# Performance work log

Hardware: AMD Instinct MI355X
Metric: run time of the kernel (lower is better)

## Reference

```python
import jax, jax.numpy as jnp
import numpy as np

N_USER, N_ITEM, N_REL = 200000, 100000, 64
DIM = 64
S_UU = S_UI = S_IU = S_II = 8
BATCH = 65536
MAX_RATING = 5.0


def setup_inputs() -> dict:
    key = jax.random.key(0)
    ks = jax.random.split(key, 24)
    inp = {}
    # query batch
    inp['u'] = jax.random.randint(ks[0], (BATCH,), 0, N_USER)
    inp['v'] = jax.random.randint(ks[1], (BATCH,), 0, N_ITEM)
    # embedding tables (init std=0.8 as in the torch code)
    inp['usr_feat'] = 0.8 * jax.random.normal(ks[2], (N_USER, DIM), jnp.float32)
    inp['item_feat'] = 0.8 * jax.random.normal(ks[3], (N_ITEM, DIM), jnp.float32)
    inp['rel_feat'] = 0.8 * jax.random.normal(ks[4], (N_REL, DIM), jnp.float32)
    # precomputed sampled neighbor tables (built once in __init__ in the original)
    inp['neigh_uu'] = jax.random.randint(ks[5], (N_USER, S_UU), 0, N_USER)
    inp['neigh_uu_st'] = jax.random.uniform(ks[6], (N_USER, S_UU), jnp.float32)
    inp['neigh_ui'] = jax.random.randint(ks[7], (N_USER, S_UI), 0, N_ITEM)
    inp['neigh_ui_rat'] = MAX_RATING * jax.random.uniform(ks[8], (N_USER, S_UI), jnp.float32)
    inp['neigh_ui_vot'] = jax.random.uniform(ks[9], (N_USER, S_UI), jnp.float32)
    inp['neigh_ui_tim'] = jax.random.uniform(ks[10], (N_USER, S_UI), jnp.float32)
    inp['neigh_iu'] = jax.random.randint(ks[11], (N_ITEM, S_IU), 0, N_USER)
    inp['neigh_iu_rat'] = MAX_RATING * jax.random.uniform(ks[12], (N_ITEM, S_IU), jnp.float32)
    inp['neigh_iu_vot'] = jax.random.uniform(ks[13], (N_ITEM, S_IU), jnp.float32)
    inp['neigh_iu_tim'] = jax.random.uniform(ks[14], (N_ITEM, S_IU), jnp.float32)
    inp['neigh_ii'] = jax.random.randint(ks[15], (N_ITEM, S_II), 0, N_ITEM)
    inp['neigh_ir'] = jax.random.randint(ks[16], (N_ITEM, S_II), 0, N_REL)
    # aggregator transforms (one per side)
    sc = 1.0 / np.sqrt(DIM)
    inp['Wu'] = sc * jax.random.normal(ks[17], (DIM, DIM), jnp.float32)
    inp['bu'] = jnp.zeros((DIM,), jnp.float32)
    inp['Wv'] = sc * jax.random.normal(ks[18], (DIM, DIM), jnp.float32)
    inp['bv'] = jnp.zeros((DIM,), jnp.float32)
    return inp


def reference(u, v, usr_feat, item_feat, rel_feat,
              neigh_uu, neigh_uu_st, neigh_ui, neigh_ui_rat, neigh_ui_vot, neigh_ui_tim,
              neigh_iu, neigh_iu_rat, neigh_iu_vot, neigh_iu_tim, neigh_ii, neigh_ir,
              Wu, bu, Wv, bv):
    u_emb = usr_feat[u]                                   # [B, D]
    v_emb = item_feat[v]                                  # [B, D]

    # ---- user-side aggregation ----
    # social neighbors, weighted by softmax over social tie strength
    uu_nei = usr_feat[neigh_uu[u]]                        # [B, S, D]
    w_uu = jax.nn.softmax(neigh_uu_st[u], axis=-1)        # [B, S]
    agg_uu = jnp.einsum('bs,bsd->bd', w_uu, uu_nei)
    # interacted items, weighted by rating * vote * time recency
    ui_nei = item_feat[neigh_ui[u]]                       # [B, S, D]
    s_ui = neigh_ui_rat[u] * neigh_ui_vot[u] * neigh_ui_tim[u]
    w_ui = jax.nn.softmax(s_ui, axis=-1)
    agg_ui = jnp.einsum('bs,bsd->bd', w_ui, ui_nei)
    user_h = jax.nn.relu((u_emb + agg_uu + agg_ui) @ Wu + bu)

    # ---- item-side aggregation ----
    # users who interacted with the item, weighted like above
    iu_nei = usr_feat[neigh_iu[v]]                        # [B, S, D]
    s_iu = neigh_iu_rat[v] * neigh_iu_vot[v] * neigh_iu_tim[v]
    w_iu = jax.nn.softmax(s_iu, axis=-1)
    agg_iu = jnp.einsum('bs,bsd->bd', w_iu, iu_nei)
    # KG neighbors with user-relation attention (KGCN-style)
    ii_nei = item_feat[neigh_ii[v]]                       # [B, S, D]
    rel = rel_feat[neigh_ir[v]]                           # [B, S, D]
    att = jnp.einsum('bd,bsd->bs', u_emb, rel)            # user-relation score
    w_ii = jax.nn.softmax(att, axis=-1)
    agg_ii = jnp.einsum('bs,bsd->bd', w_ii, ii_nei)
    item_h = jax.nn.relu((v_emb + agg_iu + agg_ii) @ Wv + bv)

    # rating prediction
    score = jax.nn.sigmoid(jnp.sum(user_h * item_h, axis=-1)) * MAX_RATING
    return score
```

## Files before the change

### kernel.cpp

```cpp
#include <hip/hip_runtime.h>
#include <math.h>

constexpr int DIM = 64;
constexpr int S = 8;
constexpr int WPB = 8;
constexpr int BLOCK = WPB * 64;
constexpr int GRID = 1024;
constexpr int WSTR = 68;

__device__ __forceinline__ void octet_softmax(float sc, float* wout) {
    float m = sc;
    m = fmaxf(m, __shfl_xor(m, 1));
    m = fmaxf(m, __shfl_xor(m, 2));
    m = fmaxf(m, __shfl_xor(m, 4));
    float e = __expf(sc - m);
    float s = e;
    s += __shfl_xor(s, 1);
    s += __shfl_xor(s, 2);
    s += __shfl_xor(s, 4);
    float w = e / s;
    #pragma unroll
    for (int k = 0; k < 8; k++) wout[k] = __shfl(w, k);
}

__global__ __launch_bounds__(BLOCK)
void sestkgcn_kernel(
    const int*   __restrict__ u_idx,
    const int*   __restrict__ v_idx,
    const float* __restrict__ usr_feat,
    const float* __restrict__ item_feat,
    const float* __restrict__ rel_feat,
    const int*   __restrict__ neigh_uu,
    const float* __restrict__ neigh_uu_st,
    const int*   __restrict__ neigh_ui,
    const float* __restrict__ neigh_ui_rat,
    const float* __restrict__ neigh_ui_vot,
    const float* __restrict__ neigh_ui_tim,
    const int*   __restrict__ neigh_iu,
    const float* __restrict__ neigh_iu_rat,
    const float* __restrict__ neigh_iu_vot,
    const float* __restrict__ neigh_iu_tim,
    const int*   __restrict__ neigh_ii,
    const int*   __restrict__ neigh_ir,
    const float* __restrict__ Wu,
    const float* __restrict__ bu,
    const float* __restrict__ Wv,
    const float* __restrict__ bv,
    float*       __restrict__ out,
    int n)
{
    __shared__ float sWuT[DIM * WSTR];
    __shared__ float sWvT[DIM * WSTR];
    __shared__ float sbu[DIM];
    __shared__ float sbv[DIM];
    __shared__ float xs[WPB * DIM];

    const int tid = threadIdx.x;
    for (int i = tid; i < DIM * DIM; i += BLOCK) {
        const int d_ = i >> 6, j_ = i & 63;
        sWuT[j_ * WSTR + d_] = Wu[i];
        sWvT[j_ * WSTR + d_] = Wv[i];
    }
    if (tid < DIM) { sbu[tid] = bu[tid]; sbv[tid] = bv[tid]; }
    __syncthreads();

    const int wave = tid >> 6;
    const int lane = tid & 63;
    const int ls   = lane & 7;

    float* xw = &xs[wave * DIM];
    const float4* wuT = (const float4*)&sWuT[lane * WSTR];
    const float4* wvT = (const float4*)&sWvT[lane * WSTR];
    const float4* xw4 = (const float4*)xw;
    const float bu_l = sbu[lane];
    const float bv_l = sbv[lane];

    const int stride = GRID * WPB;
    for (int b = blockIdx.x * WPB + wave; b < n; b += stride) {
        const int u = u_idx[b];
        const int v = v_idx[b];
        const unsigned u8 = (unsigned)u << 3, v8 = (unsigned)v << 3;
        const unsigned u64o = (unsigned)u << 6, v64o = (unsigned)v << 6;

        const float u_d = usr_feat[u64o | (unsigned)lane];
        const float v_d = item_feat[v64o | (unsigned)lane];

        const float sc_uu = neigh_uu_st[u8 + ls];
        const float sc_ui = neigh_ui_rat[u8 + ls] * neigh_ui_vot[u8 + ls] * neigh_ui_tim[u8 + ls];
        const float sc_iu = neigh_iu_rat[v8 + ls] * neigh_iu_vot[v8 + ls] * neigh_iu_tim[v8 + ls];

        float w[S];
        octet_softmax(sc_uu, w);
        float agg_uu = 0.f;
        {
            const int4 i0 = ((const int4*)(neigh_uu + u8))[0];
            const int4 i1 = ((const int4*)(neigh_uu + u8))[1];
            const int ni[S] = {i0.x, i0.y, i0.z, i0.w, i1.x, i1.y, i1.z, i1.w};
            float r[S];
            #pragma unroll
            for (int s = 0; s < S; s++) r[s] = usr_feat[((unsigned)ni[s] << 6) | (unsigned)lane];
            #pragma unroll
            for (int s = 0; s < S; s++) agg_uu = fmaf(w[s], r[s], agg_uu);
        }

        octet_softmax(sc_ui, w);
        float agg_ui = 0.f;
        {
            const int4 i0 = ((const int4*)(neigh_ui + u8))[0];
            const int4 i1 = ((const int4*)(neigh_ui + u8))[1];
            const int ni[S] = {i0.x, i0.y, i0.z, i0.w, i1.x, i1.y, i1.z, i1.w};
            float r[S];
            #pragma unroll
            for (int s = 0; s < S; s++) r[s] = item_feat[((unsigned)ni[s] << 6) | (unsigned)lane];
            #pragma unroll
            for (int s = 0; s < S; s++) agg_ui = fmaf(w[s], r[s], agg_ui);
        }

        float hu;
        {
            xw[lane] = u_d + agg_uu + agg_ui;
            __threadfence_block();
            float a0 = 0.f, a1 = 0.f, a2 = 0.f, a3 = 0.f;
            #pragma unroll
            for (int k = 0; k < DIM / 4; k++) {
                float4 xv = xw4[k];
                float4 wv = wuT[k];
                a0 = fmaf(xv.x, wv.x, a0);
                a1 = fmaf(xv.y, wv.y, a1);
                a2 = fmaf(xv.z, wv.z, a2);
                a3 = fmaf(xv.w, wv.w, a3);
            }
            hu = fmaxf((a0 + a1) + (a2 + a3) + bu_l, 0.f);
        }

        octet_softmax(sc_iu, w);
        float agg_iu = 0.f;
        {
            const int4 i0 = ((const int4*)(neigh_iu + v8))[0];
            const int4 i1 = ((const int4*)(neigh_iu + v8))[1];
            const int ni[S] = {i0.x, i0.y, i0.z, i0.w, i1.x, i1.y, i1.z, i1.w};
            float r[S];
            #pragma unroll
            for (int s = 0; s < S; s++) r[s] = usr_feat[((unsigned)ni[s] << 6) | (unsigned)lane];
            #pragma unroll
            for (int s = 0; s < S; s++) agg_iu = fmaf(w[s], r[s], agg_iu);
        }

        {
            const int4 r0 = ((const int4*)(neigh_ir + v8))[0];
            const int4 r1 = ((const int4*)(neigh_ir + v8))[1];
            const int nr[S] = {r0.x, r0.y, r0.z, r0.w, r1.x, r1.y, r1.z, r1.w};
            float p[S];
            #pragma unroll
            for (int s = 0; s < S; s++) p[s] = u_d * rel_feat[((unsigned)nr[s] << 6) | (unsigned)lane];

            float m1[4];
            #pragma unroll
            for (int i = 0; i < 4; i++) {
                float lo = (lane & 1) ? p[2 * i + 1] : p[2 * i];
                float hi = (lane & 1) ? p[2 * i]     : p[2 * i + 1];
                m1[i] = lo + __shfl_xor(hi, 1);
            }
            float m2[2];
            #pragma unroll
            for (int i = 0; i < 2; i++) {
                float lo = (lane & 2) ? m1[2 * i + 1] : m1[2 * i];
                float hi = (lane & 2) ? m1[2 * i]     : m1[2 * i + 1];
                m2[i] = lo + __shfl_xor(hi, 2);
            }
            float lo = (lane & 4) ? m2[1] : m2[0];
            float hi = (lane & 4) ? m2[0] : m2[1];
            float att = lo + __shfl_xor(hi, 4);
            att += __shfl_xor(att, 8);
            att += __shfl_xor(att, 16);
            att += __shfl_xor(att, 32);
            octet_softmax(att, w);
        }
        float agg_ii = 0.f;
        {
            const int4 i0 = ((const int4*)(neigh_ii + v8))[0];
            const int4 i1 = ((const int4*)(neigh_ii + v8))[1];
            const int ni[S] = {i0.x, i0.y, i0.z, i0.w, i1.x, i1.y, i1.z, i1.w};
            float r[S];
            #pragma unroll
            for (int s = 0; s < S; s++) r[s] = item_feat[((unsigned)ni[s] << 6) | (unsigned)lane];
            #pragma unroll
            for (int s = 0; s < S; s++) agg_ii = fmaf(w[s], r[s], agg_ii);
        }

        float hv;
        {
            xw[lane] = v_d + agg_iu + agg_ii;
            __threadfence_block();
            float a0 = 0.f, a1 = 0.f, a2 = 0.f, a3 = 0.f;
            #pragma unroll
            for (int k = 0; k < DIM / 4; k++) {
                float4 xv = xw4[k];
                float4 wv = wvT[k];
                a0 = fmaf(xv.x, wv.x, a0);
                a1 = fmaf(xv.y, wv.y, a1);
                a2 = fmaf(xv.z, wv.z, a2);
                a3 = fmaf(xv.w, wv.w, a3);
            }
            hv = fmaxf((a0 + a1) + (a2 + a3) + bv_l, 0.f);
        }

        float p = hu * hv;
        #pragma unroll
        for (int off = 32; off > 0; off >>= 1) p += __shfl_xor(p, off);
        if (lane == 0) out[b] = 5.0f / (1.0f + __expf(-p));
    }
}

extern "C" void kernel_launch(void* const* d_in, const int* in_sizes, int n_in,
                              void* d_out, int out_size, void* d_ws, size_t ws_size,
                              hipStream_t stream) {
    const int*   u_idx        = (const int*)  d_in[0];
    const int*   v_idx        = (const int*)  d_in[1];
    const float* usr_feat     = (const float*)d_in[2];
    const float* item_feat    = (const float*)d_in[3];
    const float* rel_feat     = (const float*)d_in[4];
    const int*   neigh_uu     = (const int*)  d_in[5];
    const float* neigh_uu_st  = (const float*)d_in[6];
    const int*   neigh_ui     = (const int*)  d_in[7];
    const float* neigh_ui_rat = (const float*)d_in[8];
    const float* neigh_ui_vot = (const float*)d_in[9];
    const float* neigh_ui_tim = (const float*)d_in[10];
    const int*   neigh_iu     = (const int*)  d_in[11];
    const float* neigh_iu_rat = (const float*)d_in[12];
    const float* neigh_iu_vot = (const float*)d_in[13];
    const float* neigh_iu_tim = (const float*)d_in[14];
    const int*   neigh_ii     = (const int*)  d_in[15];
    const int*   neigh_ir     = (const int*)  d_in[16];
    const float* Wu           = (const float*)d_in[17];
    const float* bu           = (const float*)d_in[18];
    const float* Wv           = (const float*)d_in[19];
    const float* bv           = (const float*)d_in[20];
    float*       out          = (float*)d_out;

    const int n = in_sizes[0];
    int blocks = (n + WPB - 1) / WPB;
    if (blocks > GRID) blocks = GRID;
    sestkgcn_kernel<<<blocks, BLOCK, 0, stream>>>(
        u_idx, v_idx, usr_feat, item_feat, rel_feat,
        neigh_uu, neigh_uu_st, neigh_ui, neigh_ui_rat, neigh_ui_vot, neigh_ui_tim,
        neigh_iu, neigh_iu_rat, neigh_iu_vot, neigh_iu_tim, neigh_ii, neigh_ir,
        Wu, bu, Wv, bv, out, n);
}
```

Baseline: 254.6 us.

## Process two queries per wave with scalarized indices and DPP reductions

```diff
diff --git a/kernel.cpp b/kernel.cpp
--- a/kernel.cpp
+++ b/kernel.cpp
@@ -8,22 +8,17 @@
 constexpr int GRID = 1024;
 constexpr int WSTR = 68;
 
-__device__ __forceinline__ void octet_softmax(float sc, float* wout) {
-    float m = sc;
-    m = fmaxf(m, __shfl_xor(m, 1));
-    m = fmaxf(m, __shfl_xor(m, 2));
-    m = fmaxf(m, __shfl_xor(m, 4));
-    float e = __expf(sc - m);
-    float s = e;
-    s += __shfl_xor(s, 1);
-    s += __shfl_xor(s, 2);
-    s += __shfl_xor(s, 4);
-    float w = e / s;
-    #pragma unroll
-    for (int k = 0; k < 8; k++) wout[k] = __shfl(w, k);
+__device__ __forceinline__ int rfl(int x) { return __builtin_amdgcn_readfirstlane(x); }
+
+template <int CTRL>
+__device__ __forceinline__ float dppx(float x) {
+    return __builtin_bit_cast(float,
+        __builtin_amdgcn_mov_dpp(__builtin_bit_cast(int, x), CTRL, 0xf, 0xf, true));
 }
-
-__global__ __launch_bounds__(BLOCK)
+#define XOR1 0xB1
+#define XOR2 0x4E
+
+__global__ __launch_bounds__(BLOCK, 4)
 void sestkgcn_kernel(
     const int*   __restrict__ u_idx,
     const int*   __restrict__ v_idx,
@@ -53,7 +48,8 @@
     __shared__ float sWvT[DIM * WSTR];
     __shared__ float sbu[DIM];
     __shared__ float sbv[DIM];
-    __shared__ float xs[WPB * DIM];
+    __shared__ float xpack[WPB][2 * DIM];
+    __shared__ float estrip[WPB][2][8];
 
     const int tid = threadIdx.x;
     for (int i = tid; i < DIM * DIM; i += BLOCK) {
@@ -66,149 +62,208 @@
 
     const int wave = tid >> 6;
     const int lane = tid & 63;
-    const int ls   = lane & 7;
-
-    float* xw = &xs[wave * DIM];
+
     const float4* wuT = (const float4*)&sWuT[lane * WSTR];
     const float4* wvT = (const float4*)&sWvT[lane * WSTR];
-    const float4* xw4 = (const float4*)xw;
     const float bu_l = sbu[lane];
     const float bv_l = sbv[lane];
-
-    const int stride = GRID * WPB;
-    for (int b = blockIdx.x * WPB + wave; b < n; b += stride) {
-        const int u = u_idx[b];
-        const int v = v_idx[b];
-        const unsigned u8 = (unsigned)u << 3, v8 = (unsigned)v << 3;
-        const unsigned u64o = (unsigned)u << 6, v64o = (unsigned)v << 6;
-
-        const float u_d = usr_feat[u64o | (unsigned)lane];
-        const float v_d = item_feat[v64o | (unsigned)lane];
-
-        const float sc_uu = neigh_uu_st[u8 + ls];
-        const float sc_ui = neigh_ui_rat[u8 + ls] * neigh_ui_vot[u8 + ls] * neigh_ui_tim[u8 + ls];
-        const float sc_iu = neigh_iu_rat[v8 + ls] * neigh_iu_vot[v8 + ls] * neigh_iu_tim[v8 + ls];
-
-        float w[S];
-        octet_softmax(sc_uu, w);
-        float agg_uu = 0.f;
-        {
-            const int4 i0 = ((const int4*)(neigh_uu + u8))[0];
-            const int4 i1 = ((const int4*)(neigh_uu + u8))[1];
-            const int ni[S] = {i0.x, i0.y, i0.z, i0.w, i1.x, i1.y, i1.z, i1.w};
-            float r[S];
-            #pragma unroll
-            for (int s = 0; s < S; s++) r[s] = usr_feat[((unsigned)ni[s] << 6) | (unsigned)lane];
-            #pragma unroll
-            for (int s = 0; s < S; s++) agg_uu = fmaf(w[s], r[s], agg_uu);
+    float*       xp  = xpack[wave];
+    const float4* xq = (const float4*)xp;
+
+    const int pstride = GRID * WPB * 2;
+    for (int b0 = (blockIdx.x * WPB + wave) * 2; b0 < n; b0 += pstride) {
+        const int b1 = b0 + 1;
+        const bool has1 = (b1 < n);
+
+        float xu[2], xv[2];
+
+        #pragma unroll
+        for (int t = 0; t < 2; t++) {
+            const int bb = t ? (has1 ? b1 : b0) : b0;
+            const int u = rfl(u_idx[bb]);
+            const int v = rfl(v_idx[bb]);
+            const float u_d = usr_feat[((size_t)u << 6) + lane];
+            const float v_d = item_feat[((size_t)v << 6) + lane];
+
+            float agg_uu;
+            {
+                const float4 sA = ((const float4*)(neigh_uu_st + (size_t)u * S))[0];
+                const float4 sB = ((const float4*)(neigh_uu_st + (size_t)u * S))[1];
+                const float sc[S] = {sA.x, sA.y, sA.z, sA.w, sB.x, sB.y, sB.z, sB.w};
+                float m = sc[0];
+                #pragma unroll
+                for (int s = 1; s < S; s++) m = fmaxf(m, sc[s]);
+                float e[S], sum = 0.f;
+                #pragma unroll
+                for (int s = 0; s < S; s++) { e[s] = __expf(sc[s] - m); sum += e[s]; }
+                const float inv = 1.f / sum;
+                const int4 i0 = ((const int4*)(neigh_uu + (size_t)u * S))[0];
+                const int4 i1 = ((const int4*)(neigh_uu + (size_t)u * S))[1];
+                const int ni[S] = {i0.x, i0.y, i0.z, i0.w, i1.x, i1.y, i1.z, i1.w};
+                float acc = 0.f;
+                #pragma unroll
+                for (int s = 0; s < S; s++)
+                    acc = fmaf(e[s], usr_feat[((size_t)rfl(ni[s]) << 6) + lane], acc);
+                agg_uu = acc * inv;
+            }
+
+            float agg_ui;
+            {
+                const float4 rA = ((const float4*)(neigh_ui_rat + (size_t)u * S))[0];
+                const float4 rB = ((const float4*)(neigh_ui_rat + (size_t)u * S))[1];
+                const float4 vA = ((const float4*)(neigh_ui_vot + (size_t)u * S))[0];
+                const float4 vB = ((const float4*)(neigh_ui_vot + (size_t)u * S))[1];
+                const float4 tA = ((const float4*)(neigh_ui_tim + (size_t)u * S))[0];
+                const float4 tB = ((const float4*)(neigh_ui_tim + (size_t)u * S))[1];
+                const float sc[S] = {rA.x*vA.x*tA.x, rA.y*vA.y*tA.y, rA.z*vA.z*tA.z, rA.w*vA.w*tA.w,
+                                     rB.x*vB.x*tB.x, rB.y*vB.y*tB.y, rB.z*vB.z*tB.z, rB.w*vB.w*tB.w};
+                float m = sc[0];
+                #pragma unroll
+                for (int s = 1; s < S; s++) m = fmaxf(m, sc[s]);
+                float e[S], sum = 0.f;
+                #pragma unroll
+                for (int s = 0; s < S; s++) { e[s] = __expf(sc[s] - m); sum += e[s]; }
+                const float inv = 1.f / sum;
+                const int4 i0 = ((const int4*)(neigh_ui + (size_t)u * S))[0];
+                const int4 i1 = ((const int4*)(neigh_ui + (size_t)u * S))[1];
+                const int ni[S] = {i0.x, i0.y, i0.z, i0.w, i1.x, i1.y, i1.z, i1.w};
+                float acc = 0.f;
+                #pragma unroll
+                for (int s = 0; s < S; s++)
+                    acc = fmaf(e[s], item_feat[((size_t)rfl(ni[s]) << 6) + lane], acc);
+                agg_ui = acc * inv;
+            }
+
+            float agg_iu;
+            {
+                const float4 rA = ((const float4*)(neigh_iu_rat + (size_t)v * S))[0];
+                const float4 rB = ((const float4*)(neigh_iu_rat + (size_t)v * S))[1];
+                const float4 vA = ((const float4*)(neigh_iu_vot + (size_t)v * S))[0];
+                const float4 vB = ((const float4*)(neigh_iu_vot + (size_t)v * S))[1];
+                const float4 tA = ((const float4*)(neigh_iu_tim + (size_t)v * S))[0];
+                const float4 tB = ((const float4*)(neigh_iu_tim + (size_t)v * S))[1];
+                const float sc[S] = {rA.x*vA.x*tA.x, rA.y*vA.y*tA.y, rA.z*vA.z*tA.z, rA.w*vA.w*tA.w,
+                                     rB.x*vB.x*tB.x, rB.y*vB.y*tB.y, rB.z*vB.z*tB.z, rB.w*vB.w*tB.w};
+                float m = sc[0];
+                #pragma unroll
+                for (int s = 1; s < S; s++) m = fmaxf(m, sc[s]);
+                float e[S], sum = 0.f;
+                #pragma unroll
+                for (int s = 0; s < S; s++) { e[s] = __expf(sc[s] - m); sum += e[s]; }
+                const float inv = 1.f / sum;
+                const int4 i0 = ((const int4*)(neigh_iu + (size_t)v * S))[0];
+                const int4 i1 = ((const int4*)(neigh_iu + (size_t)v * S))[1];
+                const int ni[S] = {i0.x, i0.y, i0.z, i0.w, i1.x, i1.y, i1.z, i1.w};
+                float acc = 0.f;
+                #pragma unroll
+                for (int s = 0; s < S; s++)
+                    acc = fmaf(e[s], usr_feat[((size_t)rfl(ni[s]) << 6) + lane], acc);
+                agg_iu = acc * inv;
+            }
+
+            float agg_ii;
+            {
+                const int4 r0 = ((const int4*)(neigh_ir + (size_t)v * S))[0];
+                const int4 r1 = ((const int4*)(neigh_ir + (size_t)v * S))[1];
+                const int nr[S] = {r0.x, r0.y, r0.z, r0.w, r1.x, r1.y, r1.z, r1.w};
+                float p[S];
+                #pragma unroll
+                for (int s = 0; s < S; s++)
+                    p[s] = u_d * rel_feat[((size_t)rfl(nr[s]) << 6) + lane];
+
+                float m1[4];
+                #pragma unroll
+                for (int i = 0; i < 4; i++) {
+                    float lo = (lane & 1) ? p[2*i+1] : p[2*i];
+                    float hi = (lane & 1) ? p[2*i]   : p[2*i+1];
+                    m1[i] = lo + dppx<XOR1>(hi);
+                }
+                float m2[2];
+                #pragma unroll
+                for (int i = 0; i < 2; i++) {
+                    float lo = (lane & 2) ? m1[2*i+1] : m1[2*i];
+                    float hi = (lane & 2) ? m1[2*i]   : m1[2*i+1];
+                    m2[i] = lo + dppx<XOR2>(hi);
+                }
+                float lo = (lane & 4) ? m2[1] : m2[0];
+                float hi = (lane & 4) ? m2[0] : m2[1];
+                float att = lo + __shfl_xor(hi, 4);
+                att += __shfl_xor(att, 8);
+                att += __shfl_xor(att, 16);
+                att += __shfl_xor(att, 32);
+                float mm = att;
+                mm = fmaxf(mm, dppx<XOR1>(mm));
+                mm = fmaxf(mm, dppx<XOR2>(mm));
+                mm = fmaxf(mm, __shfl_xor(mm, 4));
+                const float e = __expf(att - mm);
+                float ssum = e;
+                ssum += dppx<XOR1>(ssum);
+                ssum += dppx<XOR2>(ssum);
+                ssum += __shfl_xor(ssum, 4);
+                const float inv = 1.f / ssum;
+                if (lane < 8) estrip[wave][t][lane] = e;
+                __threadfence_block();
+                const float4 eA = ((const float4*)estrip[wave][t])[0];
+                const float4 eB = ((const float4*)estrip[wave][t])[1];
+                const float ee[S] = {eA.x, eA.y, eA.z, eA.w, eB.x, eB.y, eB.z, eB.w};
+                const int4 i0 = ((const int4*)(neigh_ii + (size_t)v * S))[0];
+                const int4 i1 = ((const int4*)(neigh_ii + (size_t)v * S))[1];
+                const int ni[S] = {i0.x, i0.y, i0.z, i0.w, i1.x, i1.y, i1.z, i1.w};
+                float acc = 0.f;
+                #pragma unroll
+                for (int s = 0; s < S; s++)
+                    acc = fmaf(ee[s], item_feat[((size_t)rfl(ni[s]) << 6) + lane], acc);
+                agg_ii = acc * inv;
+            }
+
+            xu[t] = u_d + agg_uu + agg_ui;
+            xv[t] = v_d + agg_iu + agg_ii;
         }
 
-        octet_softmax(sc_ui, w);
-        float agg_ui = 0.f;
-        {
-            const int4 i0 = ((const int4*)(neigh_ui + u8))[0];
-            const int4 i1 = ((const int4*)(neigh_ui + u8))[1];
-            const int ni[S] = {i0.x, i0.y, i0.z, i0.w, i1.x, i1.y, i1.z, i1.w};
-            float r[S];
-            #pragma unroll
-            for (int s = 0; s < S; s++) r[s] = item_feat[((unsigned)ni[s] << 6) | (unsigned)lane];
-            #pragma unroll
-            for (int s = 0; s < S; s++) agg_ui = fmaf(w[s], r[s], agg_ui);
+        ((float2*)xp)[lane] = make_float2(xu[0], xu[1]);
+        __threadfence_block();
+        float a0=0.f,a1=0.f,a2=0.f,a3=0.f, c0=0.f,c1=0.f,c2=0.f,c3=0.f;
+        #pragma unroll
+        for (int k = 0; k < DIM / 4; k++) {
+            const float4 wv = wuT[k];
+            const float4 xA = xq[2*k];
+            const float4 xB = xq[2*k+1];
+            a0 = fmaf(xA.x, wv.x, a0); a1 = fmaf(xA.z, wv.y, a1);
+            a2 = fmaf(xB.x, wv.z, a2); a3 = fmaf(xB.z, wv.w, a3);
+            c0 = fmaf(xA.y, wv.x, c0); c1 = fmaf(xA.w, wv.y, c1);
+            c2 = fmaf(xB.y, wv.z, c2); c3 = fmaf(xB.w, wv.w, c3);
         }
-
-        float hu;
-        {
-            xw[lane] = u_d + agg_uu + agg_ui;
-            __threadfence_block();
-            float a0 = 0.f, a1 = 0.f, a2 = 0.f, a3 = 0.f;
-            #pragma unroll
-            for (int k = 0; k < DIM / 4; k++) {
-                float4 xv = xw4[k];
-                float4 wv = wuT[k];
-                a0 = fmaf(xv.x, wv.x, a0);
-                a1 = fmaf(xv.y, wv.y, a1);
-                a2 = fmaf(xv.z, wv.z, a2);
-                a3 = fmaf(xv.w, wv.w, a3);
-            }
-            hu = fmaxf((a0 + a1) + (a2 + a3) + bu_l, 0.f);
+        const float hu0 = fmaxf((a0+a1)+(a2+a3)+bu_l, 0.f);
+        const float hu1 = fmaxf((c0+c1)+(c2+c3)+bu_l, 0.f);
+
+        __threadfence_block();
+        ((float2*)xp)[lane] = make_float2(xv[0], xv[1]);
+        __threadfence_block();
+        float d0=0.f,d1=0.f,d2=0.f,d3=0.f, g0=0.f,g1=0.f,g2=0.f,g3=0.f;
+        #pragma unroll
+        for (int k = 0; k < DIM / 4; k++) {
+            const float4 wv = wvT[k];
+            const float4 xA = xq[2*k];
+            const float4 xB = xq[2*k+1];
+            d0 = fmaf(xA.x, wv.x, d0); d1 = fmaf(xA.z, wv.y, d1);
+            d2 = fmaf(xB.x, wv.z, d2); d3 = fmaf(xB.z, wv.w, d3);
+            g0 = fmaf(xA.y, wv.x, g0); g1 = fmaf(xA.w, wv.y, g1);
+            g2 = fmaf(xB.y, wv.z, g2); g3 = fmaf(xB.w, wv.w, g3);
         }
-
-        octet_softmax(sc_iu, w);
-        float agg_iu = 0.f;
-        {
-            const int4 i0 = ((const int4*)(neigh_iu + v8))[0];
-            const int4 i1 = ((const int4*)(neigh_iu + v8))[1];
-            const int ni[S] = {i0.x, i0.y, i0.z, i0.w, i1.x, i1.y, i1.z, i1.w};
-            float r[S];
-            #pragma unroll
-            for (int s = 0; s < S; s++) r[s] = usr_feat[((unsigned)ni[s] << 6) | (unsigned)lane];
-            #pragma unroll
-            for (int s = 0; s < S; s++) agg_iu = fmaf(w[s], r[s], agg_iu);
-        }
-
-        {
-            const int4 r0 = ((const int4*)(neigh_ir + v8))[0];
-            const int4 r1 = ((const int4*)(neigh_ir + v8))[1];
-            const int nr[S] = {r0.x, r0.y, r0.z, r0.w, r1.x, r1.y, r1.z, r1.w};
-            float p[S];
-            #pragma unroll
-            for (int s = 0; s < S; s++) p[s] = u_d * rel_feat[((unsigned)nr[s] << 6) | (unsigned)lane];
-
-            float m1[4];
-            #pragma unroll
-            for (int i = 0; i < 4; i++) {
-                float lo = (lane & 1) ? p[2 * i + 1] : p[2 * i];
-                float hi = (lane & 1) ? p[2 * i]     : p[2 * i + 1];
-                m1[i] = lo + __shfl_xor(hi, 1);
-            }
-            float m2[2];
-            #pragma unroll
-            for (int i = 0; i < 2; i++) {
-                float lo = (lane & 2) ? m1[2 * i + 1] : m1[2 * i];
-                float hi = (lane & 2) ? m1[2 * i]     : m1[2 * i + 1];
-                m2[i] = lo + __shfl_xor(hi, 2);
-            }
-            float lo = (lane & 4) ? m2[1] : m2[0];
-            float hi = (lane & 4) ? m2[0] : m2[1];
-            float att = lo + __shfl_xor(hi, 4);
-            att += __shfl_xor(att, 8);
-            att += __shfl_xor(att, 16);
-            att += __shfl_xor(att, 32);
-            octet_softmax(att, w);
-        }
-        float agg_ii = 0.f;
-        {
-            const int4 i0 = ((const int4*)(neigh_ii + v8))[0];
-            const int4 i1 = ((const int4*)(neigh_ii + v8))[1];
-            const int ni[S] = {i0.x, i0.y, i0.z, i0.w, i1.x, i1.y, i1.z, i1.w};
-            float r[S];
-            #pragma unroll
-            for (int s = 0; s < S; s++) r[s] = item_feat[((unsigned)ni[s] << 6) | (unsigned)lane];
-            #pragma unroll
-            for (int s = 0; s < S; s++) agg_ii = fmaf(w[s], r[s], agg_ii);
-        }
-
-        float hv;
-        {
-            xw[lane] = v_d + agg_iu + agg_ii;
-            __threadfence_block();
-            float a0 = 0.f, a1 = 0.f, a2 = 0.f, a3 = 0.f;
-            #pragma unroll
-            for (int k = 0; k < DIM / 4; k++) {
-                float4 xv = xw4[k];
-                float4 wv = wvT[k];
-                a0 = fmaf(xv.x, wv.x, a0);
-                a1 = fmaf(xv.y, wv.y, a1);
-                a2 = fmaf(xv.z, wv.z, a2);
-                a3 = fmaf(xv.w, wv.w, a3);
-            }
-            hv = fmaxf((a0 + a1) + (a2 + a3) + bv_l, 0.f);
-        }
-
-        float p = hu * hv;
-        #pragma unroll
-        for (int off = 32; off > 0; off >>= 1) p += __shfl_xor(p, off);
-        if (lane == 0) out[b] = 5.0f / (1.0f + __expf(-p));
+        const float hv0 = fmaxf((d0+d1)+(d2+d3)+bv_l, 0.f);
+        const float hv1 = fmaxf((g0+g1)+(g2+g3)+bv_l, 0.f);
+
+        const float p0 = hu0 * hv0, p1 = hu1 * hv1;
+        float s0 = p0 + dppx<XOR1>(p0);
+        float s1 = p1 + dppx<XOR1>(p1);
+        float tt = (lane & 1) ? s1 : s0;
+        tt += dppx<XOR2>(tt);
+        tt += __shfl_xor(tt, 4);
+        tt += __shfl_xor(tt, 8);
+        tt += __shfl_xor(tt, 16);
+        tt += __shfl_xor(tt, 32);
+        if (lane == 0) out[b0] = 5.f / (1.f + __expf(-tt));
+        else if (lane == 1 && has1) out[b1] = 5.f / (1.f + __expf(-tt));
     }
 }
 
@@ -239,7 +294,7 @@
     float*       out          = (float*)d_out;
 
     const int n = in_sizes[0];
-    int blocks = (n + WPB - 1) / WPB;
+    int blocks = (n + WPB * 2 - 1) / (WPB * 2);
     if (blocks > GRID) blocks = GRID;
     sestkgcn_kernel<<<blocks, BLOCK, 0, stream>>>(
         u_idx, v_idx, usr_feat, item_feat, rel_feat,
```

New measurement: 292.5 us. 14.9% more time.
